# Performance work log

Hardware: AMD Instinct MI355X
Metric: run time of the kernel (lower is better)

The kernel has to match this reference:

```python
import jax, jax.numpy as jnp
import numpy as np

N_USERS, N_ITEMS = 100000, 50000
N_EDGES, N_PAIRS = 1000000, 500000
D_IN, D_HID, D_OUT = 128, 128, 64
EPS = 1e-12


def _mean_agg(h_src, src, dst, n_dst):
    # gather src features along edges, scatter-sum to dst, divide by in-degree
    msg = h_src[src]                                            # [E, d]
    s = jax.ops.segment_sum(msg, dst, num_segments=n_dst)       # [n_dst, d]
    deg = jax.ops.segment_sum(jnp.ones(src.shape, h_src.dtype), dst, num_segments=n_dst)
    return s / jnp.maximum(deg, 1.0)[:, None]


def _conv(h_src, h_dst, src, dst, n_dst, Wn, bn, Ws, bs):
    # SAGE-mean style ConvLayer: fc_neigh(mean) + fc_self(dst), ReLU, L2 norm
    hn = _mean_agg(h_src, src, dst, n_dst)
    z = hn @ Wn + bn + h_dst @ Ws + bs
    z = jax.nn.relu(z)
    return z / jnp.maximum(jnp.linalg.norm(z, axis=-1, keepdims=True), EPS)


def _l2n(x):
    return x / jnp.maximum(jnp.linalg.norm(x, axis=-1, keepdims=True), EPS)


def setup_inputs() -> dict:
    key = jax.random.key(0)
    ks = jax.random.split(key, 20)
    f = lambda k, shp: (jax.random.normal(k, shp, jnp.float32) * 0.05)
    ri = lambda k, shp, hi: jax.random.randint(k, shp, 0, hi, jnp.int32)
    return {
        'h_user': jax.random.normal(ks[0], (N_USERS, D_IN), jnp.float32),
        'h_item': jax.random.normal(ks[1], (N_ITEMS, D_IN), jnp.float32),
        'Wn01': f(ks[2], (2, 2, D_HID, D_HID)),
        'bn01': f(ks[3], (2, 2, D_HID)),
        'Ws01': f(ks[4], (2, 2, D_HID, D_HID)),
        'bs01': f(ks[5], (2, 2, D_HID)),
        'Wn2': f(ks[6], (2, D_HID, D_OUT)),
        'bn2': f(ks[7], (2, D_OUT)),
        'Ws2': f(ks[8], (2, D_HID, D_OUT)),
        'bs2': f(ks[9], (2, D_OUT)),
        'u2i_src': ri(ks[10], (N_EDGES,), N_USERS),
        'u2i_dst': ri(ks[11], (N_EDGES,), N_ITEMS),
        'i2u_src': ri(ks[12], (N_EDGES,), N_ITEMS),
        'i2u_dst': ri(ks[13], (N_EDGES,), N_USERS),
        'pos_u': ri(ks[14], (N_PAIRS,), N_USERS),
        'pos_i': ri(ks[15], (N_PAIRS,), N_ITEMS),
        'neg_u': ri(ks[16], (N_PAIRS,), N_USERS),
        'neg_i': ri(ks[17], (N_PAIRS,), N_ITEMS),
    }


def reference(h_user, h_item, Wn01, bn01, Ws01, bs01, Wn2, bn2, Ws2, bs2,
              u2i_src, u2i_dst, i2u_src, i2u_dst, pos_u, pos_i, neg_u, neg_i):
    n_users, n_items = h_user.shape[0], h_item.shape[0]
    hu, hi = h_user, h_item
    # layers 0,1: etype 0 = user->item ('rates'), etype 1 = item->user (reverse)
    for l in range(2):
        hi_new = _conv(hu, hi, u2i_src, u2i_dst, n_items,
                       Wn01[l, 0], bn01[l, 0], Ws01[l, 0], bs01[l, 0])
        hu_new = _conv(hi, hu, i2u_src, i2u_dst, n_users,
                       Wn01[l, 1], bn01[l, 1], Ws01[l, 1], bs01[l, 1])
        hu, hi = hu_new, hi_new
    # layer 2: hidden -> out
    hi_new = _conv(hu, hi, u2i_src, u2i_dst, n_items, Wn2[0], bn2[0], Ws2[0], bs2[0])
    hu_new = _conv(hi, hu, i2u_src, i2u_dst, n_users, Wn2[1], bn2[1], Ws2[1], bs2[1])
    hu, hi = hu_new, hi_new
    # CosinePrediction on pos/neg graphs (user -rates-> item edges)
    nu, ni = _l2n(hu), _l2n(hi)
    pos_score = jnp.sum(nu[pos_u] * ni[pos_i], axis=-1)
    neg_score = jnp.sum(nu[neg_u] * ni[neg_i], axis=-1)
    return hu, hi, pos_score, neg_score
```

## Files before the change

kernel.cpp:

```cpp
#include <hip/hip_runtime.h>
#include <hip/hip_bf16.h>

#define NU 100000
#define NI 50000
#define NE 1000000
#define NP 500000

#define GIB 12500
#define GUB 25000
#define AGG_GRID 50000

typedef unsigned short u16;
typedef unsigned int u32;
typedef __attribute__((ext_vector_type(8))) short short8;
typedef __attribute__((ext_vector_type(4))) float f32x4;

static __device__ __forceinline__ u16 f2bf(float f) {
    union { float f; u32 u; } x; x.f = f;
    u32 r = x.u + 0x7fff + ((x.u >> 16) & 1);
    return (u16)(r >> 16);
}
static __device__ __forceinline__ float bf2f(u16 h) {
    union { u32 u; float f; } x; x.u = ((u32)h) << 16;
    return x.f;
}

__global__ __launch_bounds__(256) void cvt_kernel(const float* __restrict__ in,
                                                  u16* __restrict__ out, int n8) {
    int i = blockIdx.x * blockDim.x + threadIdx.x;
    if (i >= n8) return;
    float4 a = ((const float4*)in)[2 * i];
    float4 b = ((const float4*)in)[2 * i + 1];
    ushort4 lo = {f2bf(a.x), f2bf(a.y), f2bf(a.z), f2bf(a.w)};
    ushort4 hi = {f2bf(b.x), f2bf(b.y), f2bf(b.z), f2bf(b.w)};
    ((ushort4*)out)[2 * i]     = lo;
    ((ushort4*)out)[2 * i + 1] = hi;
}

__global__ void wtrans_all_kernel(const float* __restrict__ Wn01,
                                  const float* __restrict__ Ws01,
                                  const float* __restrict__ Wn2,
                                  const float* __restrict__ Ws2,
                                  u16* __restrict__ wt) {
    int x = blockIdx.x;
    int k = threadIdx.x;
    if (x < 512) {
        int m = x >> 7, n = x & 127;
        const float* Wn = Wn01 + m * 16384;
        const float* Ws = Ws01 + m * 16384;
        size_t o = (size_t)m * 128 * 256;
        wt[o + (size_t)n * 256 + k]       = f2bf(Wn[(size_t)k * 128 + n]);
        wt[o + (size_t)n * 256 + 128 + k] = f2bf(Ws[(size_t)k * 128 + n]);
    } else {
        int m = (x - 512) >> 7;
        int n = (x - 512) & 127;
        size_t o = 131072 + (size_t)m * 16384;
        float v;
        if (m == 0) v = (n < 64) ? Wn2[(size_t)k * 64 + n]
                                 : Ws2[8192 + (size_t)k * 64 + (n - 64)];
        else        v = (n < 64) ? Wn2[8192 + (size_t)k * 64 + n]
                                 : Ws2[(size_t)k * 64 + (n - 64)];
        wt[o + (size_t)n * 128 + k] = f2bf(v);
    }
}


__global__ void hist2_kernel(const int* __restrict__ d0, int* __restrict__ deg0,
                             int* __restrict__ rank0,
                             const int* __restrict__ d1, int* __restrict__ deg1,
                             int* __restrict__ rank1, int E) {
    int e = blockIdx.x * blockDim.x + threadIdx.x;
    if (e >= E) return;
    if (blockIdx.y == 0) {
        int d = __builtin_nontemporal_load(&d0[e]);
        int r = atomicAdd(&deg0[d], 1);
        __builtin_nontemporal_store(r, &rank0[e]);
    } else {
        int d = __builtin_nontemporal_load(&d1[e]);
        int r = atomicAdd(&deg1[d], 1);
        __builtin_nontemporal_store(r, &rank1[e]);
    }
}

__global__ void scan2_local_kernel(const int* __restrict__ in0, int* __restrict__ out0,
                                   int* __restrict__ bsum0, int n0,
                                   const int* __restrict__ in1, int* __restrict__ out1,
                                   int* __restrict__ bsum1, int n1) {
    const int* in; int *out, *bsum; int n;
    if (blockIdx.y == 0) { in = in0; out = out0; bsum = bsum0; n = n0; }
    else                 { in = in1; out = out1; bsum = bsum1; n = n1; }
    __shared__ int s[1024];
    int i = blockIdx.x * 1024 + threadIdx.x;
    int v = (i < n) ? in[i] : 0;
    s[threadIdx.x] = v;
    __syncthreads();
    for (int off = 1; off < 1024; off <<= 1) {
        int t = (threadIdx.x >= off) ? s[threadIdx.x - off] : 0;
        __syncthreads();
        s[threadIdx.x] += t;
        __syncthreads();
    }
    if (i < n) out[i] = s[threadIdx.x] - v;
    if (threadIdx.x == 1023) bsum[blockIdx.x] = s[1023];
}

__global__ void scan2_bsum_kernel(int* b0, int nb0, int* b1, int nb1) {
    int* bsum; int nb;
    if (blockIdx.y == 0) { bsum = b0; nb = nb0; }
    else                 { bsum = b1; nb = nb1; }
    __shared__ int s[1024];
    int v = ((int)threadIdx.x < nb) ? bsum[threadIdx.x] : 0;
    s[threadIdx.x] = v;
    __syncthreads();
    for (int off = 1; off < 1024; off <<= 1) {
        int t = (threadIdx.x >= off) ? s[threadIdx.x - off] : 0;
        __syncthreads();
        s[threadIdx.x] += t;
        __syncthreads();
    }
    if ((int)threadIdx.x < nb) bsum[threadIdx.x] = s[threadIdx.x] - v;
}

__global__ void scan2_finalize_kernel(int* __restrict__ rs0, const int* __restrict__ b0,
                                      int n0, int* __restrict__ rs1,
                                      const int* __restrict__ b1, int n1, int E) {
    int* rs; const int* bsum; int n;
    if (blockIdx.y == 0) { rs = rs0; bsum = b0; n = n0; }
    else                 { rs = rs1; bsum = b1; n = n1; }
    int i = blockIdx.x * 1024 + threadIdx.x;
    if (i < n) rs[i] += bsum[blockIdx.x];
    if (i == 0) rs[n] = E;
}

__global__ void fill2_kernel(const int* __restrict__ s0, const int* __restrict__ d0,
                             const int* __restrict__ r0, const int* __restrict__ rs0,
                             int* __restrict__ csr0,
                             const int* __restrict__ s1, const int* __restrict__ d1,
                             const int* __restrict__ r1, const int* __restrict__ rs1,
                             int* __restrict__ csr1, int E) {
    const int *src, *dst, *rk, *rs; int* csr;
    if (blockIdx.y == 0) { src = s0; dst = d0; rk = r0; rs = rs0; csr = csr0; }
    else                 { src = s1; dst = d1; rk = r1; rs = rs1; csr = csr1; }
    int e = blockIdx.x * blockDim.x + threadIdx.x;
    if (e >= E) return;
    int d = __builtin_nontemporal_load(&dst[e]);
    int r = __builtin_nontemporal_load(&rk[e]);
    int s = __builtin_nontemporal_load(&src[e]);
    csr[rs[d] + r] = s;
}

__global__ __launch_bounds__(256) void agg2_kernel(
    const u16* __restrict__ hu, const u16* __restrict__ hi,
    const int* __restrict__ rs_i, const int* __restrict__ csr_i,
    u16* __restrict__ out_i,
    const int* __restrict__ rs_u, const int* __restrict__ csr_u,
    u16* __restrict__ out_u) {
    const u16* hsrc; const int *rs, *csr; u16* out; int T, blk;
    int base = blockIdx.x >> 3, r8 = blockIdx.x & 7;
    if (r8 < 4) { blk = base * 4 + r8;
                  if (blk >= GIB) return;
                  hsrc = hu; rs = rs_i; csr = csr_i; out = out_i; T = NI; }
    else        { blk = base * 4 + (r8 - 4);
                  if (blk >= GUB) return;
                  hsrc = hi; rs = rs_u; csr = csr_u; out = out_u; T = NU; }
    int t = blk * 4 + (threadIdx.x >> 6);
    if (t >= T) return;
    const int lane = threadIdx.x & 63;
    const int lr   = lane & 15;
    const int sub  = lane >> 4;
    int e0 = rs[t], e1 = rs[t + 1];
    float acc[8] = {};
    int e = e0 + sub;
    for (; e + 12 < e1; e += 16) {
        int s0 = __builtin_nontemporal_load(&csr[e]);
        int s1 = __builtin_nontemporal_load(&csr[e + 4]);
        int s2 = __builtin_nontemporal_load(&csr[e + 8]);
        int s3 = __builtin_nontemporal_load(&csr[e + 12]);
        short8 v0 = *(const short8*)&hsrc[(size_t)s0 * 128 + (lr << 3)];
        short8 v1 = *(const short8*)&hsrc[(size_t)s1 * 128 + (lr << 3)];
        short8 v2 = *(const short8*)&hsrc[(size_t)s2 * 128 + (lr << 3)];
        short8 v3 = *(const short8*)&hsrc[(size_t)s3 * 128 + (lr << 3)];
        #pragma unroll
        for (int q = 0; q < 8; ++q)
            acc[q] += (bf2f((u16)v0[q]) + bf2f((u16)v1[q])) +
                      (bf2f((u16)v2[q]) + bf2f((u16)v3[q]));
    }
    for (; e + 4 < e1; e += 8) {
        int s0 = __builtin_nontemporal_load(&csr[e]);
        int s1 = __builtin_nontemporal_load(&csr[e + 4]);
        short8 v0 = *(const short8*)&hsrc[(size_t)s0 * 128 + (lr << 3)];
        short8 v1 = *(const short8*)&hsrc[(size_t)s1 * 128 + (lr << 3)];
        #pragma unroll
        for (int q = 0; q < 8; ++q)
            acc[q] += bf2f((u16)v0[q]) + bf2f((u16)v1[q]);
    }
    if (e < e1) {
        int s0 = __builtin_nontemporal_load(&csr[e]);
        short8 v0 = *(const short8*)&hsrc[(size_t)s0 * 128 + (lr << 3)];
        #pragma unroll
        for (int q = 0; q < 8; ++q) acc[q] += bf2f((u16)v0[q]);
    }
    #pragma unroll
    for (int q = 0; q < 8; ++q) {
        acc[q] += __shfl_xor(acc[q], 16);
        acc[q] += __shfl_xor(acc[q], 32);
    }
    if (sub == 0) {
        float inv = (e1 > e0) ? 1.f / (float)(e1 - e0) : 0.f;
        short8 o;
        #pragma unroll
        for (int q = 0; q < 8; ++q) o[q] = (short)f2bf(acc[q] * inv);
        __builtin_nontemporal_store(o, (short8*)&out[(size_t)t * 128 + (lr << 3)]);
    }
}

__global__ __launch_bounds__(256) void agg64_kernel(
    const u16* __restrict__ pu, const u16* __restrict__ pi,
    const int* __restrict__ rs_i, const int* __restrict__ csr_i,
    u16* __restrict__ out_i,
    const int* __restrict__ rs_u, const int* __restrict__ csr_u,
    u16* __restrict__ out_u) {
    const u16* hsrc; const int *rs, *csr; u16* out; int T, blk;
    int base = blockIdx.x >> 3, r8 = blockIdx.x & 7;
    if (r8 < 4) { blk = base * 4 + r8;
                  if (blk >= GIB) return;
                  hsrc = pu; rs = rs_i; csr = csr_i; out = out_i; T = NI; }
    else        { blk = base * 4 + (r8 - 4);
                  if (blk >= GUB) return;
                  hsrc = pi; rs = rs_u; csr = csr_u; out = out_u; T = NU; }
    int t = blk * 4 + (threadIdx.x >> 6);
    if (t >= T) return;
    const int lane = threadIdx.x & 63;
    const int lr   = lane & 7;
    const int sub  = lane >> 3;
    int e0 = rs[t], e1 = rs[t + 1];
    float acc[8] = {};
    int e = e0 + sub;
    for (; e + 8 < e1; e += 16) {
        int s0 = __builtin_nontemporal_load(&csr[e]);
        int s1 = __builtin_nontemporal_load(&csr[e + 8]);
        short8 v0 = *(const short8*)&hsrc[(size_t)s0 * 128 + (lr << 3)];
        short8 v1 = *(const short8*)&hsrc[(size_t)s1 * 128 + (lr << 3)];
        #pragma unroll
        for (int q = 0; q < 8; ++q)
            acc[q] += bf2f((u16)v0[q]) + bf2f((u16)v1[q]);
    }
    if (e < e1) {
        int s0 = __builtin_nontemporal_load(&csr[e]);
        short8 v0 = *(const short8*)&hsrc[(size_t)s0 * 128 + (lr << 3)];
        #pragma unroll
        for (int q = 0; q < 8; ++q) acc[q] += bf2f((u16)v0[q]);
    }
    #pragma unroll
    for (int q = 0; q < 8; ++q) {
        acc[q] += __shfl_xor(acc[q], 8);
        acc[q] += __shfl_xor(acc[q], 16);
        acc[q] += __shfl_xor(acc[q], 32);
    }
    if (sub == 0) {
        float inv = (e1 > e0) ? 1.f / (float)(e1 - e0) : 0.f;
        short8 o;
        #pragma unroll
        for (int q = 0; q < 8; ++q) o[q] = (short)f2bf(acc[q] * inv);
        __builtin_nontemporal_store(o, (short8*)&out[(size_t)t * 64 + (lr << 3)]);
    }
}

__global__ __launch_bounds__(256) void conv2_kernel(
    const u16* __restrict__ hn_i, const u16* __restrict__ hd_i,
    const u16* __restrict__ wt_i, const float* __restrict__ bn_i,
    const float* __restrict__ bs_i, u16* __restrict__ outb_i, int ci,
    const u16* __restrict__ hn_u, const u16* __restrict__ hd_u,
    const u16* __restrict__ wt_u, const float* __restrict__ bn_u,
    const float* __restrict__ bs_u, u16* __restrict__ outb_u)
{
    constexpr int NF   = 2;
    constexpr int FSTR = 132;
    __shared__ u16 smA[64 * 264];
    __shared__ float psum[4][64];
    __shared__ float sinv[64];
    float* smF = (float*)smA;

    const u16 *hn, *hd, *Wt; const float *bn, *bs; u16* outb; int T, t0;
    if ((int)blockIdx.x < ci) {
        hn = hn_i; hd = hd_i; Wt = wt_i; bn = bn_i; bs = bs_i;
        outb = outb_i; T = NI; t0 = blockIdx.x * 64;
    } else {
        hn = hn_u; hd = hd_u; Wt = wt_u; bn = bn_u; bs = bs_u;
        outb = outb_u; T = NU; t0 = (blockIdx.x - ci) * 64;
    }

    const int tid  = threadIdx.x;
    const int wave = tid >> 6;
    const int lane = tid & 63;
    const int lr   = lane & 15;
    const int lg   = lane >> 4;

    #pragma unroll
    for (int i = 0; i < 8; ++i) {
        int lin = i * 256 + tid;
        int row = lin >> 5;
        int q   = lin & 31;
        int t   = t0 + row; if (t >= T) t = T - 1;
        const u16* srcp = (q < 16) ? &hn[(size_t)t * 128 + (q << 3)]
                                   : &hd[(size_t)t * 128 + ((q - 16) << 3)];
        *(short8*)&smA[row * 264 + (q << 3)] = *(const short8*)srcp;
    }
    __syncthreads();

    const u16* wp[NF];
    float bias[NF];
    #pragma unroll
    for (int ni = 0; ni < NF; ++ni) {
        int col = wave * 32 + ni * 16 + lr;
        wp[ni] = Wt + (size_t)col * 256;
        bias[ni] = bn[col] + bs[col];
    }

    f32x4 acc[4][NF];
    #pragma unroll
    for (int mi = 0; mi < 4; ++mi)
        #pragma unroll
        for (int ni = 0; ni < NF; ++ni)
            acc[mi][ni] = (f32x4){0.f, 0.f, 0.f, 0.f};

    #pragma unroll
    for (int ks = 0; ks < 8; ++ks) {
        const int kb = ks * 32 + (lg << 3);
        short8 b[NF];
        #pragma unroll
        for (int ni = 0; ni < NF; ++ni) b[ni] = *(const short8*)&wp[ni][kb];
        #pragma unroll
        for (int mi = 0; mi < 4; ++mi) {
            short8 a = *(const short8*)&smA[(mi * 16 + lr) * 264 + kb];
            #pragma unroll
            for (int ni = 0; ni < NF; ++ni)
                acc[mi][ni] = __builtin_amdgcn_mfma_f32_16x16x32_bf16(a, b[ni], acc[mi][ni], 0, 0, 0);
        }
    }
    __syncthreads();

    float rsum[4][4];
    #pragma unroll
    for (int mi = 0; mi < 4; ++mi) {
        #pragma unroll
        for (int j = 0; j < 4; ++j) {
            int rowg = mi * 16 + lg * 4 + j;
            float s = 0.f;
            #pragma unroll
            for (int ni = 0; ni < NF; ++ni) {
                float z = fmaxf(acc[mi][ni][j] + bias[ni], 0.f);
                int colg = wave * 32 + ni * 16 + lr;
                smF[rowg * FSTR + colg] = z;
                s = fmaf(z, z, s);
            }
            rsum[mi][j] = s;
        }
    }
    #pragma unroll
    for (int m = 1; m < 16; m <<= 1)
        #pragma unroll
        for (int mi = 0; mi < 4; ++mi)
            #pragma unroll
            for (int j = 0; j < 4; ++j)
                rsum[mi][j] += __shfl_xor(rsum[mi][j], m);
    if (lr == 0) {
        #pragma unroll
        for (int mi = 0; mi < 4; ++mi)
            #pragma unroll
            for (int j = 0; j < 4; ++j)
                psum[wave][mi * 16 + lg * 4 + j] = rsum[mi][j];
    }
    __syncthreads();
    if (tid < 64) {
        float n2 = psum[0][tid] + psum[1][tid] + psum[2][tid] + psum[3][tid];
        sinv[tid] = 1.f / fmaxf(sqrtf(n2), 1e-12f);
    }
    __syncthreads();

    #pragma unroll
    for (int i = 0; i < 4; ++i) {
        int lin = i * 256 + tid;
        int row = lin >> 4, g = lin & 15;
        int t = t0 + row;
        if (t < T) {
            float inv = sinv[row];
            float4 z0 = *(float4*)&smF[row * FSTR + g * 8];
            float4 z1 = *(float4*)&smF[row * FSTR + g * 8 + 4];
            short8 ob = {(short)f2bf(z0.x * inv), (short)f2bf(z0.y * inv),
                         (short)f2bf(z0.z * inv), (short)f2bf(z0.w * inv),
                         (short)f2bf(z1.x * inv), (short)f2bf(z1.y * inv),
                         (short)f2bf(z1.z * inv), (short)f2bf(z1.w * inv)};
            *(short8*)&outb[(size_t)t * 128 + g * 8] = ob;
        }
    }
}

__global__ __launch_bounds__(256) void proj2_kernel(
    const u16* __restrict__ A_i, const u16* __restrict__ wt_pi,
    u16* __restrict__ out_i, int ci,
    const u16* __restrict__ A_u, const u16* __restrict__ wt_pu,
    u16* __restrict__ out_u)
{
    constexpr int NF = 2;
    constexpr int FSTR = 132;
    __shared__ float smF[64 * FSTR];
    u16* smA = (u16*)smF;

    const u16 *A, *Wt; u16* outb; int T, t0;
    if ((int)blockIdx.x < ci) {
        A = A_i; Wt = wt_pi; outb = out_i; T = NI; t0 = blockIdx.x * 64;
    } else {
        A = A_u; Wt = wt_pu; outb = out_u; T = NU; t0 = (blockIdx.x - ci) * 64;
    }

    const int tid  = threadIdx.x;
    const int wave = tid >> 6;
    const int lane = tid & 63;
    const int lr   = lane & 15;
    const int lg   = lane >> 4;

    #pragma unroll
    for (int i = 0; i < 4; ++i) {
        int lin = i * 256 + tid;
        int row = lin >> 4;
        int q   = lin & 15;
        int t   = t0 + row; if (t >= T) t = T - 1;
        *(short8*)&smA[row * 136 + (q << 3)] =
            *(const short8*)&A[(size_t)t * 128 + (q << 3)];
    }
    __syncthreads();

    const u16* wp[NF];
    #pragma unroll
    for (int ni = 0; ni < NF; ++ni) {
        int col = wave * 32 + ni * 16 + lr;
        wp[ni] = Wt + (size_t)col * 128;
    }

    f32x4 acc[4][NF];
    #pragma unroll
    for (int mi = 0; mi < 4; ++mi)
        #pragma unroll
        for (int ni = 0; ni < NF; ++ni)
            acc[mi][ni] = (f32x4){0.f, 0.f, 0.f, 0.f};

    #pragma unroll
    for (int ks = 0; ks < 4; ++ks) {
        const int kb = ks * 32 + (lg << 3);
        short8 b[NF];
        #pragma unroll
        for (int ni = 0; ni < NF; ++ni) b[ni] = *(const short8*)&wp[ni][kb];
        #pragma unroll
        for (int mi = 0; mi < 4; ++mi) {
            short8 a = *(const short8*)&smA[(mi * 16 + lr) * 136 + kb];
            #pragma unroll
            for (int ni = 0; ni < NF; ++ni)
                acc[mi][ni] = __builtin_amdgcn_mfma_f32_16x16x32_bf16(a, b[ni], acc[mi][ni], 0, 0, 0);
        }
    }
    __syncthreads();

    #pragma unroll
    for (int mi = 0; mi < 4; ++mi)
        #pragma unroll
        for (int j = 0; j < 4; ++j) {
            int rowg = mi * 16 + lg * 4 + j;
            #pragma unroll
            for (int ni = 0; ni < NF; ++ni)
                smF[rowg * FSTR + wave * 32 + ni * 16 + lr] = acc[mi][ni][j];
        }
    __syncthreads();

    #pragma unroll
    for (int i = 0; i < 4; ++i) {
        int lin = i * 256 + tid;
        int row = lin >> 4, g = lin & 15;
        int t = t0 + row;
        if (t < T) {
            float4 z0 = *(float4*)&smF[row * FSTR + g * 8];
            float4 z1 = *(float4*)&smF[row * FSTR + g * 8 + 4];
            short8 ob = {(short)f2bf(z0.x), (short)f2bf(z0.y),
                         (short)f2bf(z0.z), (short)f2bf(z0.w),
                         (short)f2bf(z1.x), (short)f2bf(z1.y),
                         (short)f2bf(z1.z), (short)f2bf(z1.w)};
            *(short8*)&outb[(size_t)t * 128 + g * 8] = ob;
        }
    }
}

__global__ __launch_bounds__(256) void combine2_kernel(
    const u16* __restrict__ agg_i, const u16* __restrict__ proj_i,
    const float* __restrict__ bn2, const float* __restrict__ bs2,
    float* __restrict__ outf_i, u16* __restrict__ outb_i, int cbi,
    const u16* __restrict__ agg_u, const u16* __restrict__ proj_u,
    float* __restrict__ outf_u, u16* __restrict__ outb_u)
{
    const u16 *agg, *proj; const float *bn, *bs; float* outf; u16* outb; int T, r0;
    if ((int)blockIdx.x < cbi) {
        agg = agg_i; proj = proj_i; bn = bn2;      bs = bs2;
        outf = outf_i; outb = outb_i; T = NI; r0 = blockIdx.x * 32;
    } else {
        agg = agg_u; proj = proj_u; bn = bn2 + 64; bs = bs2 + 64;
        outf = outf_u; outb = outb_u; T = NU; r0 = (blockIdx.x - cbi) * 32;
    }
    int g = threadIdx.x >> 3, l = threadIdx.x & 7;
    int r = r0 + g;
    if (r >= T) return;
    short8 va = *(const short8*)&agg[(size_t)r * 64 + (l << 3)];
    short8 vs = *(const short8*)&proj[(size_t)r * 128 + 64 + (l << 3)];
    float z[8];
    float s = 0.f;
    #pragma unroll
    for (int q = 0; q < 8; ++q) {
        float v = bf2f((u16)va[q]) + bf2f((u16)vs[q]) + bn[l * 8 + q] + bs[l * 8 + q];
        v = fmaxf(v, 0.f);
        z[q] = v;
        s = fmaf(v, v, s);
    }
    s += __shfl_xor(s, 1);
    s += __shfl_xor(s, 2);
    s += __shfl_xor(s, 4);
    float inv = 1.f / fmaxf(sqrtf(s), 1e-12f);
    short8 ob;
    float4 o0, o1;
    o0.x = z[0] * inv; o0.y = z[1] * inv; o0.z = z[2] * inv; o0.w = z[3] * inv;
    o1.x = z[4] * inv; o1.y = z[5] * inv; o1.z = z[6] * inv; o1.w = z[7] * inv;
    #pragma unroll
    for (int q = 0; q < 8; ++q) ob[q] = (short)f2bf(z[q] * inv);
    *(short8*)&outb[(size_t)r * 64 + (l << 3)] = ob;
    *(float4*)&outf[(size_t)r * 64 + (l << 3)]     = o0;
    *(float4*)&outf[(size_t)r * 64 + (l << 3) + 4] = o1;
}

__global__ __launch_bounds__(256) void score2_kernel(
    const u16* __restrict__ hu, const u16* __restrict__ hi,
    const int* __restrict__ pu0, const int* __restrict__ pi0, float* __restrict__ out0,
    const int* __restrict__ pu1, const int* __restrict__ pi1, float* __restrict__ out1,
    int P) {
    const int *pu, *pi; float* out;
    if (blockIdx.y == 0) { pu = pu0; pi = pi0; out = out0; }
    else                 { pu = pu1; pi = pi1; out = out1; }
    int g = threadIdx.x >> 3, l = threadIdx.x & 7;
    int p = blockIdx.x * 32 + g;
    if (p >= P) return;
    int u = __builtin_nontemporal_load(&pu[p]);
    int it = __builtin_nontemporal_load(&pi[p]);
    short8 a = *(const short8*)&hu[(size_t)u * 64 + (l << 3)];
    short8 b = *(const short8*)&hi[(size_t)it * 64 + (l << 3)];
    float d = 0.f, na = 0.f, nb = 0.f;
    #pragma unroll
    for (int q = 0; q < 8; ++q) {
        float x = bf2f((u16)a[q]), y = bf2f((u16)b[q]);
        d  = fmaf(x, y, d);
        na = fmaf(x, x, na);
        nb = fmaf(y, y, nb);
    }
    #pragma unroll
    for (int m = 1; m < 8; m <<= 1) {
        d  += __shfl_xor(d, m);
        na += __shfl_xor(na, m);
        nb += __shfl_xor(nb, m);
    }
    if (l == 0) out[p] = d / (fmaxf(sqrtf(na), 1e-12f) * fmaxf(sqrtf(nb), 1e-12f));
}


extern "C" void kernel_launch(void* const* d_in, const int* in_sizes, int n_in,
                              void* d_out, int out_size, void* d_ws, size_t ws_size,
                              hipStream_t stream) {
    const float* h_user = (const float*)d_in[0];
    const float* h_item = (const float*)d_in[1];
    const float* Wn01   = (const float*)d_in[2];
    const float* bn01   = (const float*)d_in[3];
    const float* Ws01   = (const float*)d_in[4];
    const float* bs01   = (const float*)d_in[5];
    const float* Wn2    = (const float*)d_in[6];
    const float* bn2    = (const float*)d_in[7];
    const float* Ws2    = (const float*)d_in[8];
    const float* bs2    = (const float*)d_in[9];
    const int* u2i_src  = (const int*)d_in[10];
    const int* u2i_dst  = (const int*)d_in[11];
    const int* i2u_src  = (const int*)d_in[12];
    const int* i2u_dst  = (const int*)d_in[13];
    const int* pos_u    = (const int*)d_in[14];
    const int* pos_i    = (const int*)d_in[15];
    const int* neg_u    = (const int*)d_in[16];
    const int* neg_i    = (const int*)d_in[17];

    float* out = (float*)d_out;
    float* out_hu = out;
    float* out_hi = out + (size_t)NU * 64;
    float* out_pos = out + (size_t)NU * 64 + (size_t)NI * 64;
    float* out_neg = out_pos + NP;

    char* ws = (char*)d_ws;
    size_t off = 0;
    auto alloc = [&](size_t bytes) -> void* {
        void* p = ws + off;
        off = (off + bytes + 255) & ~(size_t)255;
        return p;
    };
    u16* hu0b = (u16*)alloc((size_t)NU * 128 * 2);
    u16* hi0b = (u16*)alloc((size_t)NI * 128 * 2);
    u16* hu_b = (u16*)alloc((size_t)NU * 128 * 2);
    u16* hi_b = (u16*)alloc((size_t)NI * 128 * 2);
    u16* hu_a = (u16*)alloc((size_t)NU * 128 * 2);
    u16* hi_a = (u16*)alloc((size_t)NI * 128 * 2);
    u16* agg_i = (u16*)alloc((size_t)NI * 128 * 2);
    u16* agg_u = (u16*)alloc((size_t)NU * 128 * 2);
    u16* hu2b = (u16*)alloc((size_t)NU * 64 * 2);
    u16* hi2b = (u16*)alloc((size_t)NI * 64 * 2);
    u16* wt_all = (u16*)alloc((size_t)(4 * 128 * 256 + 2 * 128 * 128) * 2);
    u16* wt_l0_i = wt_all;
    u16* wt_l0_u = wt_all + 32768;
    u16* wt_l1_i = wt_all + 65536;
    u16* wt_l1_u = wt_all + 98304;
    u16* wt_pu   = wt_all + 131072;
    u16* wt_pi   = wt_all + 147456;
    int* csr_u2i = (int*)alloc((size_t)NE * 4);
    int* csr_i2u = (int*)alloc((size_t)NE * 4);
    int* rs_i   = (int*)alloc((size_t)(NI + 1) * 4);
    int* rs_u   = (int*)alloc((size_t)(NU + 1) * 4);
    int* deg    = (int*)alloc((size_t)(NI + NU) * 4);
    int* bsum_i = (int*)alloc(1024 * 4);
    int* bsum_u = (int*)alloc(1024 * 4);
    int* deg_i = deg, *deg_u = deg + NI;
    int* rank_i = (int*)agg_i;
    int* rank_u = (int*)agg_u;
    u16* proj_u = hu_b;
    u16* proj_i = hi_b;
    u16* agg64_i = agg_i;
    u16* agg64_u = agg_u;
    (void)ws_size; (void)in_sizes; (void)n_in; (void)out_size;

    const int eblocks = (NE + 255) / 256;

    cvt_kernel<<<(NU * 128 / 8 + 255) / 256, 256, 0, stream>>>(h_user, hu0b, NU * 128 / 8);
    cvt_kernel<<<(NI * 128 / 8 + 255) / 256, 256, 0, stream>>>(h_item, hi0b, NI * 128 / 8);
    wtrans_all_kernel<<<768, 128, 0, stream>>>(Wn01, Ws01, Wn2, Ws2, wt_all);

    hipMemsetAsync(deg, 0, (size_t)(NI + NU) * 4, stream);
    hist2_kernel<<<dim3(eblocks, 2), 256, 0, stream>>>(u2i_dst, deg_i, rank_i,
                                                       i2u_dst, deg_u, rank_u, NE);
    const int nb_i = (NI + 1023) / 1024, nb_u = (NU + 1023) / 1024;
    const int nb_max = (nb_i > nb_u) ? nb_i : nb_u;
    scan2_local_kernel<<<dim3(nb_max, 2), 1024, 0, stream>>>(
        deg_i, rs_i, bsum_i, NI, deg_u, rs_u, bsum_u, NU);
    scan2_bsum_kernel<<<dim3(1, 2), 1024, 0, stream>>>(bsum_i, nb_i, bsum_u, nb_u);
    scan2_finalize_kernel<<<dim3(nb_max, 2), 1024, 0, stream>>>(
        rs_i, bsum_i, NI, rs_u, bsum_u, NU, NE);
    fill2_kernel<<<dim3(eblocks, 2), 256, 0, stream>>>(
        u2i_src, u2i_dst, rank_i, rs_i, csr_u2i,
        i2u_src, i2u_dst, rank_u, rs_u, csr_i2u, NE);

    const int ci = (NI + 63) / 64, cu = (NU + 63) / 64;
    const int cbi = (NI + 31) / 32, cbu = (NU + 31) / 32;

    agg2_kernel<<<AGG_GRID, 256, 0, stream>>>(hu0b, hi0b, rs_i, csr_u2i, agg_i,
                                              rs_u, csr_i2u, agg_u);
    conv2_kernel<<<ci + cu, 256, 0, stream>>>(
        agg_i, hi0b, wt_l0_i, bn01 + 0, bs01 + 0, hi_b, ci,
        agg_u, hu0b, wt_l0_u, bn01 + 128, bs01 + 128, hu_b);
    agg2_kernel<<<AGG_GRID, 256, 0, stream>>>(hu_b, hi_b, rs_i, csr_u2i, agg_i,
                                              rs_u, csr_i2u, agg_u);
    conv2_kernel<<<ci + cu, 256, 0, stream>>>(
        agg_i, hi_b, wt_l1_i, bn01 + 256, bs01 + 256, hi_a, ci,
        agg_u, hu_b, wt_l1_u, bn01 + 384, bs01 + 384, hu_a);
    proj2_kernel<<<ci + cu, 256, 0, stream>>>(hi_a, wt_pi, proj_i, ci,
                                              hu_a, wt_pu, proj_u);
    agg64_kernel<<<AGG_GRID, 256, 0, stream>>>(proj_u, proj_i, rs_i, csr_u2i, agg64_i,
                                               rs_u, csr_i2u, agg64_u);
    combine2_kernel<<<cbi + cbu, 256, 0, stream>>>(
        agg64_i, proj_i, bn2, bs2, out_hi, hi2b, cbi,
        agg64_u, proj_u, out_hu, hu2b);

    score2_kernel<<<dim3((NP + 31) / 32, 2), 256, 0, stream>>>(
        hu2b, hi2b, pos_u, pos_i, out_pos, neg_u, neg_i, out_neg, NP);
}
```

Baseline: 581.9 us.

## Assign one 16-lane group per destination node in aggregation kernels

```diff
diff --git a/kernel.cpp b/kernel.cpp
--- a/kernel.cpp
+++ b/kernel.cpp
@@ -5,10 +5,6 @@
 #define NI 50000
 #define NE 1000000
 #define NP 500000
-
-#define GIB 12500
-#define GUB 25000
-#define AGG_GRID 50000
 
 typedef unsigned short u16;
 typedef unsigned int u32;
@@ -152,30 +148,26 @@
 __global__ __launch_bounds__(256) void agg2_kernel(
     const u16* __restrict__ hu, const u16* __restrict__ hi,
     const int* __restrict__ rs_i, const int* __restrict__ csr_i,
-    u16* __restrict__ out_i,
+    u16* __restrict__ out_i, int gi2,
     const int* __restrict__ rs_u, const int* __restrict__ csr_u,
     u16* __restrict__ out_u) {
-    const u16* hsrc; const int *rs, *csr; u16* out; int T, blk;
-    int base = blockIdx.x >> 3, r8 = blockIdx.x & 7;
-    if (r8 < 4) { blk = base * 4 + r8;
-                  if (blk >= GIB) return;
-                  hsrc = hu; rs = rs_i; csr = csr_i; out = out_i; T = NI; }
-    else        { blk = base * 4 + (r8 - 4);
-                  if (blk >= GUB) return;
-                  hsrc = hi; rs = rs_u; csr = csr_u; out = out_u; T = NU; }
-    int t = blk * 4 + (threadIdx.x >> 6);
+    const u16* hsrc; const int *rs, *csr; u16* out; int T, t;
+    int bx = blockIdx.x;
+    int grp = threadIdx.x >> 4;
+    int lr  = threadIdx.x & 15;
+    if (bx < gi2) { hsrc = hu; rs = rs_i; csr = csr_i; out = out_i; T = NI;
+                    t = bx * 16 + grp; }
+    else          { hsrc = hi; rs = rs_u; csr = csr_u; out = out_u; T = NU;
+                    t = (bx - gi2) * 16 + grp; }
     if (t >= T) return;
-    const int lane = threadIdx.x & 63;
-    const int lr   = lane & 15;
-    const int sub  = lane >> 4;
     int e0 = rs[t], e1 = rs[t + 1];
     float acc[8] = {};
-    int e = e0 + sub;
-    for (; e + 12 < e1; e += 16) {
+    int e = e0;
+    for (; e + 3 < e1; e += 4) {
         int s0 = __builtin_nontemporal_load(&csr[e]);
-        int s1 = __builtin_nontemporal_load(&csr[e + 4]);
-        int s2 = __builtin_nontemporal_load(&csr[e + 8]);
-        int s3 = __builtin_nontemporal_load(&csr[e + 12]);
+        int s1 = __builtin_nontemporal_load(&csr[e + 1]);
+        int s2 = __builtin_nontemporal_load(&csr[e + 2]);
+        int s3 = __builtin_nontemporal_load(&csr[e + 3]);
         short8 v0 = *(const short8*)&hsrc[(size_t)s0 * 128 + (lr << 3)];
         short8 v1 = *(const short8*)&hsrc[(size_t)s1 * 128 + (lr << 3)];
         short8 v2 = *(const short8*)&hsrc[(size_t)s2 * 128 + (lr << 3)];
@@ -185,85 +177,62 @@
             acc[q] += (bf2f((u16)v0[q]) + bf2f((u16)v1[q])) +
                       (bf2f((u16)v2[q]) + bf2f((u16)v3[q]));
     }
-    for (; e + 4 < e1; e += 8) {
-        int s0 = __builtin_nontemporal_load(&csr[e]);
-        int s1 = __builtin_nontemporal_load(&csr[e + 4]);
-        short8 v0 = *(const short8*)&hsrc[(size_t)s0 * 128 + (lr << 3)];
-        short8 v1 = *(const short8*)&hsrc[(size_t)s1 * 128 + (lr << 3)];
-        #pragma unroll
-        for (int q = 0; q < 8; ++q)
-            acc[q] += bf2f((u16)v0[q]) + bf2f((u16)v1[q]);
-    }
-    if (e < e1) {
+    for (; e < e1; ++e) {
         int s0 = __builtin_nontemporal_load(&csr[e]);
         short8 v0 = *(const short8*)&hsrc[(size_t)s0 * 128 + (lr << 3)];
         #pragma unroll
         for (int q = 0; q < 8; ++q) acc[q] += bf2f((u16)v0[q]);
     }
-    #pragma unroll
-    for (int q = 0; q < 8; ++q) {
-        acc[q] += __shfl_xor(acc[q], 16);
-        acc[q] += __shfl_xor(acc[q], 32);
-    }
-    if (sub == 0) {
-        float inv = (e1 > e0) ? 1.f / (float)(e1 - e0) : 0.f;
-        short8 o;
-        #pragma unroll
-        for (int q = 0; q < 8; ++q) o[q] = (short)f2bf(acc[q] * inv);
-        __builtin_nontemporal_store(o, (short8*)&out[(size_t)t * 128 + (lr << 3)]);
-    }
+    float inv = (e1 > e0) ? 1.f / (float)(e1 - e0) : 0.f;
+    short8 o;
+    #pragma unroll
+    for (int q = 0; q < 8; ++q) o[q] = (short)f2bf(acc[q] * inv);
+    __builtin_nontemporal_store(o, (short8*)&out[(size_t)t * 128 + (lr << 3)]);
 }
 
 __global__ __launch_bounds__(256) void agg64_kernel(
     const u16* __restrict__ pu, const u16* __restrict__ pi,
     const int* __restrict__ rs_i, const int* __restrict__ csr_i,
-    u16* __restrict__ out_i,
+    u16* __restrict__ out_i, int gi64,
     const int* __restrict__ rs_u, const int* __restrict__ csr_u,
     u16* __restrict__ out_u) {
-    const u16* hsrc; const int *rs, *csr; u16* out; int T, blk;
-    int base = blockIdx.x >> 3, r8 = blockIdx.x & 7;
-    if (r8 < 4) { blk = base * 4 + r8;
-                  if (blk >= GIB) return;
-                  hsrc = pu; rs = rs_i; csr = csr_i; out = out_i; T = NI; }
-    else        { blk = base * 4 + (r8 - 4);
-                  if (blk >= GUB) return;
-                  hsrc = pi; rs = rs_u; csr = csr_u; out = out_u; T = NU; }
-    int t = blk * 4 + (threadIdx.x >> 6);
+    const u16* hsrc; const int *rs, *csr; u16* out; int T, t;
+    int bx = blockIdx.x;
+    int grp = threadIdx.x >> 3;
+    int lr  = threadIdx.x & 7;
+    if (bx < gi64) { hsrc = pu; rs = rs_i; csr = csr_i; out = out_i; T = NI;
+                     t = bx * 32 + grp; }
+    else           { hsrc = pi; rs = rs_u; csr = csr_u; out = out_u; T = NU;
+                     t = (bx - gi64) * 32 + grp; }
     if (t >= T) return;
-    const int lane = threadIdx.x & 63;
-    const int lr   = lane & 7;
-    const int sub  = lane >> 3;
     int e0 = rs[t], e1 = rs[t + 1];
     float acc[8] = {};
-    int e = e0 + sub;
-    for (; e + 8 < e1; e += 16) {
+    int e = e0;
+    for (; e + 3 < e1; e += 4) {
         int s0 = __builtin_nontemporal_load(&csr[e]);
-        int s1 = __builtin_nontemporal_load(&csr[e + 8]);
+        int s1 = __builtin_nontemporal_load(&csr[e + 1]);
+        int s2 = __builtin_nontemporal_load(&csr[e + 2]);
+        int s3 = __builtin_nontemporal_load(&csr[e + 3]);
         short8 v0 = *(const short8*)&hsrc[(size_t)s0 * 128 + (lr << 3)];
         short8 v1 = *(const short8*)&hsrc[(size_t)s1 * 128 + (lr << 3)];
+        short8 v2 = *(const short8*)&hsrc[(size_t)s2 * 128 + (lr << 3)];
+        short8 v3 = *(const short8*)&hsrc[(size_t)s3 * 128 + (lr << 3)];
         #pragma unroll
         for (int q = 0; q < 8; ++q)
-            acc[q] += bf2f((u16)v0[q]) + bf2f((u16)v1[q]);
-    }
-    if (e < e1) {
+            acc[q] += (bf2f((u16)v0[q]) + bf2f((u16)v1[q])) +
+                      (bf2f((u16)v2[q]) + bf2f((u16)v3[q]));
+    }
+    for (; e < e1; ++e) {
         int s0 = __builtin_nontemporal_load(&csr[e]);
         short8 v0 = *(const short8*)&hsrc[(size_t)s0 * 128 + (lr << 3)];
         #pragma unroll
         for (int q = 0; q < 8; ++q) acc[q] += bf2f((u16)v0[q]);
     }
-    #pragma unroll
-    for (int q = 0; q < 8; ++q) {
-        acc[q] += __shfl_xor(acc[q], 8);
-        acc[q] += __shfl_xor(acc[q], 16);
-        acc[q] += __shfl_xor(acc[q], 32);
-    }
-    if (sub == 0) {
-        float inv = (e1 > e0) ? 1.f / (float)(e1 - e0) : 0.f;
-        short8 o;
-        #pragma unroll
-        for (int q = 0; q < 8; ++q) o[q] = (short)f2bf(acc[q] * inv);
-        __builtin_nontemporal_store(o, (short8*)&out[(size_t)t * 64 + (lr << 3)]);
-    }
+    float inv = (e1 > e0) ? 1.f / (float)(e1 - e0) : 0.f;
+    short8 o;
+    #pragma unroll
+    for (int q = 0; q < 8; ++q) o[q] = (short)f2bf(acc[q] * inv);
+    __builtin_nontemporal_store(o, (short8*)&out[(size_t)t * 64 + (lr << 3)]);
 }
 
 __global__ __launch_bounds__(256) void conv2_kernel(
@@ -654,23 +623,26 @@
         u2i_src, u2i_dst, rank_i, rs_i, csr_u2i,
         i2u_src, i2u_dst, rank_u, rs_u, csr_i2u, NE);
 
+    const int gi2 = (NI + 15) / 16, gu2 = (NU + 15) / 16;
+    const int gi64 = (NI + 31) / 32, gu64 = (NU + 31) / 32;
     const int ci = (NI + 63) / 64, cu = (NU + 63) / 64;
     const int cbi = (NI + 31) / 32, cbu = (NU + 31) / 32;
 
-    agg2_kernel<<<AGG_GRID, 256, 0, stream>>>(hu0b, hi0b, rs_i, csr_u2i, agg_i,
-                                              rs_u, csr_i2u, agg_u);
+    agg2_kernel<<<gi2 + gu2, 256, 0, stream>>>(hu0b, hi0b, rs_i, csr_u2i, agg_i, gi2,
+                                               rs_u, csr_i2u, agg_u);
     conv2_kernel<<<ci + cu, 256, 0, stream>>>(
         agg_i, hi0b, wt_l0_i, bn01 + 0, bs01 + 0, hi_b, ci,
         agg_u, hu0b, wt_l0_u, bn01 + 128, bs01 + 128, hu_b);
-    agg2_kernel<<<AGG_GRID, 256, 0, stream>>>(hu_b, hi_b, rs_i, csr_u2i, agg_i,
-                                              rs_u, csr_i2u, agg_u);
+    agg2_kernel<<<gi2 + gu2, 256, 0, stream>>>(hu_b, hi_b, rs_i, csr_u2i, agg_i, gi2,
+                                               rs_u, csr_i2u, agg_u);
     conv2_kernel<<<ci + cu, 256, 0, stream>>>(
         agg_i, hi_b, wt_l1_i, bn01 + 256, bs01 + 256, hi_a, ci,
         agg_u, hu_b, wt_l1_u, bn01 + 384, bs01 + 384, hu_a);
     proj2_kernel<<<ci + cu, 256, 0, stream>>>(hi_a, wt_pi, proj_i, ci,
                                               hu_a, wt_pu, proj_u);
-    agg64_kernel<<<AGG_GRID, 256, 0, stream>>>(proj_u, proj_i, rs_i, csr_u2i, agg64_i,
-                                               rs_u, csr_i2u, agg64_u);
+    agg64_kernel<<<gi64 + gu64, 256, 0, stream>>>(proj_u, proj_i, rs_i, csr_u2i,
+                                                  agg64_i, gi64,
+                                                  rs_u, csr_i2u, agg64_u);
     combine2_kernel<<<cbi + cbu, 256, 0, stream>>>(
         agg64_i, proj_i, bn2, bs2, out_hi, hi2b, cbi,
         agg64_u, proj_u, out_hu, hu2b);
```

New measurement: 503.8 us. -13.4%, faster.
